# Kernel optimization log

Hardware: AMD Instinct MI355X
Metric: run time of the kernel (lower is better)

Reference implementation:

```python
import jax, jax.numpy as jnp
import numpy as np

VOCAB = 50257
HID = 512
LABELS = 64


def setup_inputs() -> dict:
    key = jax.random.key(0)
    k1, k2, k3, k4, k5 = jax.random.split(key, 5)
    inputs = jax.random.randint(k1, (8, 4096), 0, VOCAB, dtype=jnp.int64)
    # nn.Linear(vocab_size, num_hiddens): weight [HID, VOCAB], bias [HID]
    w1 = jax.random.normal(k2, (HID, VOCAB), dtype=jnp.float32) * (1.0 / np.sqrt(VOCAB))
    b1 = jax.random.normal(k3, (HID,), dtype=jnp.float32) * 0.01
    # nn.Linear(num_hiddens, num_labels): weight [LABELS, HID], bias [LABELS]
    w2 = jax.random.normal(k4, (LABELS, HID), dtype=jnp.float32) * (1.0 / np.sqrt(HID))
    b2 = jax.random.normal(k5, (LABELS,), dtype=jnp.float32) * 0.01
    return {"inputs": inputs, "w1": w1, "b1": b1, "w2": w2, "b2": b2}


def reference(inputs, w1, b1, w2, b2):
    # one_hot(inputs) @ w1.T + b1  ==  w1.T[inputs] + b1  (exact same math)
    y = w1.T[inputs] + b1                      # [B, S, HID]
    out = jnp.einsum('bsh,lh->bsl', y, w2) + b2  # [B, S, LABELS]
    return out
```

## Files before the change

### kernel.cpp

```cpp
#include <hip/hip_runtime.h>
#include <hip/hip_bf16.h>
#include <stdint.h>

#define VOCAB 50257
#define HID 512
#define LABELS 64
#define KSPLIT 2
#define KLEN 256
#define TILEV 64
#define BP 264

typedef __attribute__((ext_vector_type(8))) short bf16x8;
typedef __attribute__((ext_vector_type(4))) float f32x4;

__device__ __forceinline__ ushort f2bf(float x) {
    uint32_t u = __float_as_uint(x);
    return (ushort)((u + 0x7fffu + ((u >> 16) & 1u)) >> 16);
}

__device__ __forceinline__ bf16x8 ld_frag(const ushort* p) {
    union { uint2 u[2]; bf16x8 v; } x;
    x.u[0] = *(const uint2*)(p);
    x.u[1] = *(const uint2*)(p + 4);
    return x.v;
}

#define MFMA_B16(a, b, c) __builtin_amdgcn_mfma_f32_16x16x32_bf16(a, b, c, 0, 0, 0)

#define PACK8(ar, dst)                                                        \
    {                                                                         \
        union { uint32_t u[4]; bf16x8 v; } _x;                                \
        _Pragma("unroll")                                                     \
        for (int j = 0; j < 4; ++j)                                           \
            _x.u[j] = (uint32_t)f2bf(ar[2 * j]) |                             \
                      ((uint32_t)f2bf(ar[2 * j + 1]) << 16);                  \
        dst = _x.v;                                                           \
    }

#define STORE_ONE(accv, m, n)                                                 \
    {                                                                         \
        int vb = v0 + wv * 32 + (m) * 16 + kg * 4;                            \
        int l  = (n) * 16 + lrow;                                             \
        _Pragma("unroll")                                                     \
        for (int rr = 0; rr < 4; ++rr)                                        \
            if (fullA || (vb + rr) < VOCAB)                                   \
                Pout[(size_t)(vb + rr) * LABELS + l] = accv[rr];              \
    }

__global__ __launch_bounds__(128) void build_mfma(
    const float* __restrict__ w1,
    const float* __restrict__ w2,
    const float* __restrict__ b1,
    const float* __restrict__ b2,
    float* __restrict__ P,
    float* __restrict__ C)
{
    const int t = threadIdx.x;

    if (blockIdx.x == (VOCAB + TILEV - 1) / TILEV) {
        if (blockIdx.y == 0 && t < LABELS) {
            float s = b2[t];
            for (int h = 0; h < HID; h += 4) {
                float4 wv4 = *(const float4*)&w2[t * HID + h];
                float4 bv4 = *(const float4*)&b1[h];
                s += wv4.x * bv4.x + wv4.y * bv4.y + wv4.z * bv4.z + wv4.w * bv4.w;
            }
            C[t] = s;
        }
        return;
    }

    __shared__ ushort lB[LABELS * BP];

    const int lane  = t & 63;
    const int wv    = t >> 6;
    const int lrow  = lane & 15;
    const int kg    = lane >> 4;
    const int v0    = blockIdx.x * TILEV;
    const int hbase = blockIdx.y * KLEN;
    float* Pout = P + (size_t)blockIdx.y * VOCAB * LABELS;
    const bool fullA = (v0 + TILEV <= VOCAB);

    const int vA0 = v0 + wv * 32 + lrow;
    const int vA1 = vA0 + 16;
    const bool ok0 = fullA || (vA0 < VOCAB);
    const bool ok1 = fullA || (vA1 < VOCAB);

#pragma unroll
    for (int i = 0; i < 32; ++i) {
        int e  = t + 128 * i;
        int l  = e >> 6;
        int hq = e & 63;
        float4 wv4 = *(const float4*)&w2[l * HID + hbase + hq * 4];
        uint32_t q0 = (uint32_t)f2bf(wv4.x) | ((uint32_t)f2bf(wv4.y) << 16);
        uint32_t q1 = (uint32_t)f2bf(wv4.z) | ((uint32_t)f2bf(wv4.w) << 16);
        *(uint32_t*)&lB[l * BP + hq * 4]     = q0;
        *(uint32_t*)&lB[l * BP + hq * 4 + 2] = q1;
    }
    __syncthreads();

    f32x4 acc00 = {0,0,0,0}, acc01 = {0,0,0,0}, acc02 = {0,0,0,0}, acc03 = {0,0,0,0};
    f32x4 acc10 = {0,0,0,0}, acc11 = {0,0,0,0}, acc12 = {0,0,0,0}, acc13 = {0,0,0,0};

#pragma unroll 2
    for (int c = 0; c < KLEN / 32; ++c) {
        float ar0[8], ar1[8];
        {
            const float* g = &w1[(size_t)(hbase + c * 32 + kg * 8) * VOCAB];
#pragma unroll
            for (int j = 0; j < 8; ++j)
                ar0[j] = ok0 ? g[(size_t)j * VOCAB + vA0] : 0.f;
#pragma unroll
            for (int j = 0; j < 8; ++j)
                ar1[j] = ok1 ? g[(size_t)j * VOCAB + vA1] : 0.f;
        }
        bf16x8 a0, a1;
        PACK8(ar0, a0);
        PACK8(ar1, a1);
        const ushort* bb = &lB[lrow * BP + c * 32 + kg * 8];
        bf16x8 b0  = ld_frag(bb);
        bf16x8 b1f = ld_frag(bb + 16 * BP);
        bf16x8 b2f = ld_frag(bb + 32 * BP);
        bf16x8 b3f = ld_frag(bb + 48 * BP);
        acc00 = MFMA_B16(a0, b0, acc00);  acc01 = MFMA_B16(a0, b1f, acc01);
        acc02 = MFMA_B16(a0, b2f, acc02); acc03 = MFMA_B16(a0, b3f, acc03);
        acc10 = MFMA_B16(a1, b0, acc10);  acc11 = MFMA_B16(a1, b1f, acc11);
        acc12 = MFMA_B16(a1, b2f, acc12); acc13 = MFMA_B16(a1, b3f, acc13);
    }

    STORE_ONE(acc00, 0, 0); STORE_ONE(acc01, 0, 1);
    STORE_ONE(acc02, 0, 2); STORE_ONE(acc03, 0, 3);
    STORE_ONE(acc10, 1, 0); STORE_ONE(acc11, 1, 1);
    STORE_ONE(acc12, 1, 2); STORE_ONE(acc13, 1, 3);
}

__global__ __launch_bounds__(256) void build_partial_folded(
    const float* __restrict__ w1,
    const float* __restrict__ b1,
    const float* __restrict__ w2,
    float* __restrict__ P,
    int klen)
{
    __shared__ float lds_a[32 * 68];
    __shared__ float lds_b[32 * 68];

    const int t     = threadIdx.x;
    const int v0    = blockIdx.x * 64;
    const int hbase = blockIdx.y * klen;
    float* Pout = P + (size_t)blockIdx.y * VOCAB * LABELS;
    const int tx = t & 15;
    const int ty = t >> 4;
    const bool full = (v0 + 64 <= VOCAB);

    float acc[4][4] = {};

    for (int h0 = hbase; h0 < hbase + klen; h0 += 32) {
#pragma unroll
        for (int i = 0; i < 8; ++i) {
            int e   = t + 256 * i;
            int row = e >> 6;
            int col = e & 63;
            int v   = v0 + col;
            float a = (full || v < VOCAB) ? w1[(size_t)(h0 + row) * VOCAB + v] : 0.f;
            lds_a[row * 68 + col] = a + b1[h0 + row];
        }
#pragma unroll
        for (int i = 0; i < 2; ++i) {
            int e   = t + 256 * i;
            int hh4 = e >> 6;
            int l   = e & 63;
            float4 bv = *(const float4*)&w2[l * HID + h0 + hh4 * 4];
            lds_b[(hh4 * 4 + 0) * 68 + l] = bv.x;
            lds_b[(hh4 * 4 + 1) * 68 + l] = bv.y;
            lds_b[(hh4 * 4 + 2) * 68 + l] = bv.z;
            lds_b[(hh4 * 4 + 3) * 68 + l] = bv.w;
        }
        __syncthreads();
#pragma unroll
        for (int hh2 = 0; hh2 < 32; ++hh2) {
            float4 a = *(const float4*)&lds_a[hh2 * 68 + tx * 4];
            float4 b = *(const float4*)&lds_b[hh2 * 68 + ty * 4];
            acc[0][0] += a.x * b.x; acc[0][1] += a.x * b.y; acc[0][2] += a.x * b.z; acc[0][3] += a.x * b.w;
            acc[1][0] += a.y * b.x; acc[1][1] += a.y * b.y; acc[1][2] += a.y * b.z; acc[1][3] += a.y * b.w;
            acc[2][0] += a.z * b.x; acc[2][1] += a.z * b.y; acc[2][2] += a.z * b.z; acc[2][3] += a.z * b.w;
            acc[3][0] += a.w * b.x; acc[3][1] += a.w * b.y; acc[3][2] += a.w * b.z; acc[3][3] += a.w * b.w;
        }
        __syncthreads();
    }

#pragma unroll
    for (int i = 0; i < 4; ++i) {
        int v = v0 + tx * 4 + i;
        if (v < VOCAB) {
            *(float4*)&Pout[(size_t)v * LABELS + ty * 4] =
                make_float4(acc[i][0], acc[i][1], acc[i][2], acc[i][3]);
        }
    }
}

__global__ __launch_bounds__(256) void gather_out(
    const int* __restrict__ idx,
    const float* __restrict__ P,
    const float* __restrict__ bias,
    float* __restrict__ out,
    int ntok, int ksplit)
{
    int g   = blockIdx.x * 256 + threadIdx.x;
    int tok = g >> 4;
    int j   = g & 15;
    if (tok >= ntok) return;
    int v = idx[tok];
    float4 s = ((const float4*)bias)[j];
    const float4* p = (const float4*)P + (size_t)v * 16 + j;
    for (int k = 0; k < ksplit; ++k) {
        float4 m = p[(size_t)k * VOCAB * 16];
        s.x += m.x; s.y += m.y; s.z += m.z; s.w += m.w;
    }
    ((float4*)out)[(size_t)tok * 16 + j] = s;
}

__global__ __launch_bounds__(256) void direct_kernel(
    const int* __restrict__ idx,
    const float* __restrict__ w1,
    const float* __restrict__ b1,
    const float* __restrict__ w2,
    const float* __restrict__ b2,
    float* __restrict__ out,
    int ntok)
{
    int g   = blockIdx.x * 256 + threadIdx.x;
    int tok = g >> 6;
    int l   = g & 63;
    if (tok >= ntok) return;
    int v = idx[tok];
    float acc = b2[l];
    for (int h = 0; h < HID; ++h)
        acc += (w1[(size_t)h * VOCAB + v] + b1[h]) * w2[l * HID + h];
    out[(size_t)tok * 64 + l] = acc;
}

extern "C" void kernel_launch(void* const* d_in, const int* in_sizes, int n_in,
                              void* d_out, int out_size, void* d_ws, size_t ws_size,
                              hipStream_t stream) {
    const int*   idx = (const int*)d_in[0];
    const float* w1  = (const float*)d_in[1];
    const float* b1  = (const float*)d_in[2];
    const float* w2  = (const float*)d_in[3];
    const float* b2  = (const float*)d_in[4];
    float* out = (float*)d_out;
    const int ntok = in_sizes[0];

    const size_t table_bytes = (size_t)VOCAB * LABELS * sizeof(float);
    const int nblk2 = (ntok * 16 + 255) / 256;

    if (ws_size >= (size_t)KSPLIT * table_bytes + 1024) {
        float* P = (float*)d_ws;
        float* C = (float*)((char*)d_ws + (size_t)KSPLIT * table_bytes);
        int ntiles = (VOCAB + TILEV - 1) / TILEV;
        dim3 grid1(ntiles + 1, KSPLIT);
        build_mfma<<<grid1, 128, 0, stream>>>(w1, w2, b1, b2, P, C);
        gather_out<<<nblk2, 256, 0, stream>>>(idx, P, C, out, ntok, KSPLIT);
    } else {
        int ksplit = 0;
        if      (ws_size >= 4 * table_bytes) ksplit = 4;
        else if (ws_size >= 2 * table_bytes) ksplit = 2;
        else if (ws_size >= 1 * table_bytes) ksplit = 1;
        if (ksplit > 0) {
            float* P = (float*)d_ws;
            dim3 grid1((VOCAB + 63) / 64, ksplit);
            build_partial_folded<<<grid1, 256, 0, stream>>>(w1, b1, w2, P, HID / ksplit);
            gather_out<<<nblk2, 256, 0, stream>>>(idx, P, b2, out, ntok, ksplit);
        } else {
            int nblk = (ntok * 64 + 255) / 256;
            direct_kernel<<<nblk, 256, 0, stream>>>(idx, w1, b1, w2, b2, out, ntok);
        }
    }
}
```

Measured before the change: 43.78 us.

## Split projection table build over labels instead of hidden dim, drop partial sums

The table build now gives each block the full hidden reduction for half of the labels, instead of half of the hidden dimension for all labels. This removes the second partial table, halving the table write and letting the gather read a single table without summation. The tradeoff is that each vocab tile of w1 is now read by two blocks, relying on L2 to avoid doubling the dominant w1 traffic. The intermediate fallback path for smaller workspaces is removed.

```diff
diff --git a/kernel.cpp b/kernel.cpp
--- a/kernel.cpp
+++ b/kernel.cpp
@@ -5,10 +5,9 @@
 #define VOCAB 50257
 #define HID 512
 #define LABELS 64
-#define KSPLIT 2
-#define KLEN 256
 #define TILEV 64
-#define BP 264
+#define NTILES ((VOCAB + TILEV - 1) / TILEV)
+#define BP 520
 
 typedef __attribute__((ext_vector_type(8))) short bf16x8;
 typedef __attribute__((ext_vector_type(4))) float f32x4;
@@ -40,11 +39,11 @@
 #define STORE_ONE(accv, m, n)                                                 \
     {                                                                         \
         int vb = v0 + wv * 32 + (m) * 16 + kg * 4;                            \
-        int l  = (n) * 16 + lrow;                                             \
+        int l  = lbase + (n) * 16 + lrow;                                     \
         _Pragma("unroll")                                                     \
         for (int rr = 0; rr < 4; ++rr)                                        \
             if (fullA || (vb + rr) < VOCAB)                                   \
-                Pout[(size_t)(vb + rr) * LABELS + l] = accv[rr];              \
+                M[(size_t)(vb + rr) * LABELS + l] = accv[rr];                 \
     }
 
 __global__ __launch_bounds__(128) void build_mfma(
@@ -52,13 +51,14 @@
     const float* __restrict__ w2,
     const float* __restrict__ b1,
     const float* __restrict__ b2,
-    float* __restrict__ P,
+    float* __restrict__ M,
     float* __restrict__ C)
 {
     const int t = threadIdx.x;
+    const int b = blockIdx.x;
 
-    if (blockIdx.x == (VOCAB + TILEV - 1) / TILEV) {
-        if (blockIdx.y == 0 && t < LABELS) {
+    if (b == 2 * NTILES) {
+        if (t < LABELS) {
             float s = b2[t];
             for (int h = 0; h < HID; h += 4) {
                 float4 wv4 = *(const float4*)&w2[t * HID + h];
@@ -70,15 +70,16 @@
         return;
     }
 
-    __shared__ ushort lB[LABELS * BP];
+    __shared__ ushort lB[32 * BP];
 
+    const int vt    = b >> 1;
+    const int lh    = b & 1;
     const int lane  = t & 63;
     const int wv    = t >> 6;
     const int lrow  = lane & 15;
     const int kg    = lane >> 4;
-    const int v0    = blockIdx.x * TILEV;
-    const int hbase = blockIdx.y * KLEN;
-    float* Pout = P + (size_t)blockIdx.y * VOCAB * LABELS;
+    const int v0    = vt * TILEV;
+    const int lbase = lh * 32;
     const bool fullA = (v0 + TILEV <= VOCAB);
 
     const int vA0 = v0 + wv * 32 + lrow;
@@ -89,9 +90,9 @@
 #pragma unroll
     for (int i = 0; i < 32; ++i) {
         int e  = t + 128 * i;
-        int l  = e >> 6;
-        int hq = e & 63;
-        float4 wv4 = *(const float4*)&w2[l * HID + hbase + hq * 4];
+        int l  = e >> 7;
+        int hq = e & 127;
+        float4 wv4 = *(const float4*)&w2[(lbase + l) * HID + hq * 4];
         uint32_t q0 = (uint32_t)f2bf(wv4.x) | ((uint32_t)f2bf(wv4.y) << 16);
         uint32_t q1 = (uint32_t)f2bf(wv4.z) | ((uint32_t)f2bf(wv4.w) << 16);
         *(uint32_t*)&lB[l * BP + hq * 4]     = q0;
@@ -99,14 +100,14 @@
     }
     __syncthreads();
 
-    f32x4 acc00 = {0,0,0,0}, acc01 = {0,0,0,0}, acc02 = {0,0,0,0}, acc03 = {0,0,0,0};
-    f32x4 acc10 = {0,0,0,0}, acc11 = {0,0,0,0}, acc12 = {0,0,0,0}, acc13 = {0,0,0,0};
+    f32x4 acc00 = {0,0,0,0}, acc01 = {0,0,0,0};
+    f32x4 acc10 = {0,0,0,0}, acc11 = {0,0,0,0};
 
 #pragma unroll 2
-    for (int c = 0; c < KLEN / 32; ++c) {
+    for (int c = 0; c < HID / 32; ++c) {
         float ar0[8], ar1[8];
         {
-            const float* g = &w1[(size_t)(hbase + c * 32 + kg * 8) * VOCAB];
+            const float* g = &w1[(size_t)(c * 32 + kg * 8) * VOCAB];
 #pragma unroll
             for (int j = 0; j < 8; ++j)
                 ar0[j] = ok0 ? g[(size_t)j * VOCAB + vA0] : 0.f;
@@ -120,90 +121,20 @@
         const ushort* bb = &lB[lrow * BP + c * 32 + kg * 8];
         bf16x8 b0  = ld_frag(bb);
         bf16x8 b1f = ld_frag(bb + 16 * BP);
-        bf16x8 b2f = ld_frag(bb + 32 * BP);
-        bf16x8 b3f = ld_frag(bb + 48 * BP);
         acc00 = MFMA_B16(a0, b0, acc00);  acc01 = MFMA_B16(a0, b1f, acc01);
-        acc02 = MFMA_B16(a0, b2f, acc02); acc03 = MFMA_B16(a0, b3f, acc03);
         acc10 = MFMA_B16(a1, b0, acc10);  acc11 = MFMA_B16(a1, b1f, acc11);
-        acc12 = MFMA_B16(a1, b2f, acc12); acc13 = MFMA_B16(a1, b3f, acc13);
     }
 
     STORE_ONE(acc00, 0, 0); STORE_ONE(acc01, 0, 1);
-    STORE_ONE(acc02, 0, 2); STORE_ONE(acc03, 0, 3);
     STORE_ONE(acc10, 1, 0); STORE_ONE(acc11, 1, 1);
-    STORE_ONE(acc12, 1, 2); STORE_ONE(acc13, 1, 3);
-}
-
-__global__ __launch_bounds__(256) void build_partial_folded(
-    const float* __restrict__ w1,
-    const float* __restrict__ b1,
-    const float* __restrict__ w2,
-    float* __restrict__ P,
-    int klen)
-{
-    __shared__ float lds_a[32 * 68];
-    __shared__ float lds_b[32 * 68];
-
-    const int t     = threadIdx.x;
-    const int v0    = blockIdx.x * 64;
-    const int hbase = blockIdx.y * klen;
-    float* Pout = P + (size_t)blockIdx.y * VOCAB * LABELS;
-    const int tx = t & 15;
-    const int ty = t >> 4;
-    const bool full = (v0 + 64 <= VOCAB);
-
-    float acc[4][4] = {};
-
-    for (int h0 = hbase; h0 < hbase + klen; h0 += 32) {
-#pragma unroll
-        for (int i = 0; i < 8; ++i) {
-            int e   = t + 256 * i;
-            int row = e >> 6;
-            int col = e & 63;
-            int v   = v0 + col;
-            float a = (full || v < VOCAB) ? w1[(size_t)(h0 + row) * VOCAB + v] : 0.f;
-            lds_a[row * 68 + col] = a + b1[h0 + row];
-        }
-#pragma unroll
-        for (int i = 0; i < 2; ++i) {
-            int e   = t + 256 * i;
-            int hh4 = e >> 6;
-            int l   = e & 63;
-            float4 bv = *(const float4*)&w2[l * HID + h0 + hh4 * 4];
-            lds_b[(hh4 * 4 + 0) * 68 + l] = bv.x;
-            lds_b[(hh4 * 4 + 1) * 68 + l] = bv.y;
-            lds_b[(hh4 * 4 + 2) * 68 + l] = bv.z;
-            lds_b[(hh4 * 4 + 3) * 68 + l] = bv.w;
-        }
-        __syncthreads();
-#pragma unroll
-        for (int hh2 = 0; hh2 < 32; ++hh2) {
-            float4 a = *(const float4*)&lds_a[hh2 * 68 + tx * 4];
-            float4 b = *(const float4*)&lds_b[hh2 * 68 + ty * 4];
-            acc[0][0] += a.x * b.x; acc[0][1] += a.x * b.y; acc[0][2] += a.x * b.z; acc[0][3] += a.x * b.w;
-            acc[1][0] += a.y * b.x; acc[1][1] += a.y * b.y; acc[1][2] += a.y * b.z; acc[1][3] += a.y * b.w;
-            acc[2][0] += a.z * b.x; acc[2][1] += a.z * b.y; acc[2][2] += a.z * b.z; acc[2][3] += a.z * b.w;
-            acc[3][0] += a.w * b.x; acc[3][1] += a.w * b.y; acc[3][2] += a.w * b.z; acc[3][3] += a.w * b.w;
-        }
-        __syncthreads();
-    }
-
-#pragma unroll
-    for (int i = 0; i < 4; ++i) {
-        int v = v0 + tx * 4 + i;
-        if (v < VOCAB) {
-            *(float4*)&Pout[(size_t)v * LABELS + ty * 4] =
-                make_float4(acc[i][0], acc[i][1], acc[i][2], acc[i][3]);
-        }
-    }
 }
 
 __global__ __launch_bounds__(256) void gather_out(
     const int* __restrict__ idx,
-    const float* __restrict__ P,
+    const float* __restrict__ M,
     const float* __restrict__ bias,
     float* __restrict__ out,
-    int ntok, int ksplit)
+    int ntok)
 {
     int g   = blockIdx.x * 256 + threadIdx.x;
     int tok = g >> 4;
@@ -211,12 +142,9 @@
     if (tok >= ntok) return;
     int v = idx[tok];
     float4 s = ((const float4*)bias)[j];
-    const float4* p = (const float4*)P + (size_t)v * 16 + j;
-    for (int k = 0; k < ksplit; ++k) {
-        float4 m = p[(size_t)k * VOCAB * 16];
-        s.x += m.x; s.y += m.y; s.z += m.z; s.w += m.w;
-    }
-    ((float4*)out)[(size_t)tok * 16 + j] = s;
+    float4 m = ((const float4*)M)[(size_t)v * 16 + j];
+    ((float4*)out)[(size_t)tok * 16 + j] =
+        make_float4(s.x + m.x, s.y + m.y, s.z + m.z, s.w + m.w);
 }
 
 __global__ __launch_bounds__(256) void direct_kernel(
@@ -253,26 +181,13 @@
     const size_t table_bytes = (size_t)VOCAB * LABELS * sizeof(float);
     const int nblk2 = (ntok * 16 + 255) / 256;
 
-    if (ws_size >= (size_t)KSPLIT * table_bytes + 1024) {
-        float* P = (float*)d_ws;
-        float* C = (float*)((char*)d_ws + (size_t)KSPLIT * table_bytes);
-        int ntiles = (VOCAB + TILEV - 1) / TILEV;
-        dim3 grid1(ntiles + 1, KSPLIT);
-        build_mfma<<<grid1, 128, 0, stream>>>(w1, w2, b1, b2, P, C);
-        gather_out<<<nblk2, 256, 0, stream>>>(idx, P, C, out, ntok, KSPLIT);
+    if (ws_size >= table_bytes + 1024) {
+        float* M = (float*)d_ws;
+        float* C = (float*)((char*)d_ws + table_bytes);
+        build_mfma<<<2 * NTILES + 1, 128, 0, stream>>>(w1, w2, b1, b2, M, C);
+        gather_out<<<nblk2, 256, 0, stream>>>(idx, M, C, out, ntok);
     } else {
-        int ksplit = 0;
-        if      (ws_size >= 4 * table_bytes) ksplit = 4;
-        else if (ws_size >= 2 * table_bytes) ksplit = 2;
-        else if (ws_size >= 1 * table_bytes) ksplit = 1;
-        if (ksplit > 0) {
-            float* P = (float*)d_ws;
-            dim3 grid1((VOCAB + 63) / 64, ksplit);
-            build_partial_folded<<<grid1, 256, 0, stream>>>(w1, b1, w2, P, HID / ksplit);
-            gather_out<<<nblk2, 256, 0, stream>>>(idx, P, b2, out, ntok, ksplit);
-        } else {
-            int nblk = (ntok * 64 + 255) / 256;
-            direct_kernel<<<nblk, 256, 0, stream>>>(idx, w1, b1, w2, b2, out, ntok);
-        }
+        int nblk = (ntok * 64 + 255) / 256;
+        direct_kernel<<<nblk, 256, 0, stream>>>(idx, w1, b1, w2, b2, out, ntok);
     }
 }
```

After: 60.20 us. 37.5% more time.
